# Performance work log

Hardware: AMD Instinct MI355X
Metric: run time of the kernel (lower is better)

The kernel has to match this reference:

```python
import jax, jax.numpy as jnp
import numpy as np

WS = 8          # window size
HEADS = 12      # attention heads
DIM = 768
HEAD_DIM = DIM // HEADS
EPS = 1e-5      # torch nn.LayerNorm default


def _layernorm(x, w, b):
    m = x.mean(-1, keepdims=True)
    v = ((x - m) ** 2).mean(-1, keepdims=True)
    return (x - m) / jnp.sqrt(v + EPS) * w + b


def setup_inputs() -> dict:
    key = jax.random.key(0)
    ks = jax.random.split(key, 8)
    s = 0.02  # weight init scale for numerical sanity
    dim, hd, ws = DIM, HEAD_DIM, WS
    return {
        "x": jax.random.normal(ks[0], (2, 16, 16, 16, dim), jnp.float32),
        "w_qkv": jax.random.normal(ks[1], (dim, 3 * dim), jnp.float32) * s,
        "b_qkv": jnp.zeros((3 * dim,), jnp.float32),
        "w_proj": jax.random.normal(ks[2], (dim, dim), jnp.float32) * s,
        "b_proj": jnp.zeros((dim,), jnp.float32),
        "rel_pos_d": jax.random.normal(ks[3], (2 * ws - 1, hd), jnp.float32) * s,
        "rel_pos_h": jax.random.normal(ks[4], (2 * ws - 1, hd), jnp.float32) * s,
        "rel_pos_w": jax.random.normal(ks[5], (2 * ws - 1, hd), jnp.float32) * s,
        "norm1_w": jnp.ones((dim,), jnp.float32),
        "norm1_b": jnp.zeros((dim,), jnp.float32),
        "norm2_w": jnp.ones((dim,), jnp.float32),
        "norm2_b": jnp.zeros((dim,), jnp.float32),
        "w1": jax.random.normal(ks[6], (dim, 4 * dim), jnp.float32) * s,
        "b1": jnp.zeros((4 * dim,), jnp.float32),
        "w2": jax.random.normal(ks[7], (4 * dim, dim), jnp.float32) * s,
        "b2": jnp.zeros((dim,), jnp.float32),
    }


def reference(x, w_qkv, b_qkv, w_proj, b_proj, rel_pos_d, rel_pos_h, rel_pos_w,
              norm1_w, norm1_b, norm2_w, norm2_b, w1, b1, w2, b2):
    B, D, H, W, C = x.shape
    ws, h = WS, HEADS
    hd = C // h
    scale = hd ** -0.5
    N = ws ** 3

    shortcut = x
    xn = _layernorm(x, norm1_w, norm1_b)

    # window partition (dims divide evenly -> no padding)
    xw = xn.reshape(B, D // ws, ws, H // ws, ws, W // ws, ws, C)
    xw = xw.transpose(0, 1, 3, 5, 2, 4, 6, 7).reshape(-1, N, C)  # [Bw, N, C]
    Bw = xw.shape[0]

    qkv = (xw @ w_qkv + b_qkv).reshape(Bw, N, 3, h, hd)
    qkv = qkv.transpose(2, 0, 3, 1, 4).reshape(3, Bw * h, N, hd)
    q, k, v = qkv[0], qkv[1], qkv[2]  # each [Bw*h, N, hd]

    attn = jnp.einsum('bqc,bkc->bqk', q * scale, k)  # [Bw*h, N, N]

    # decomposed relative position bias; q_size == k_size == ws, so no interp
    idx = jnp.arange(ws)[:, None] - jnp.arange(ws)[None, :] + (ws - 1)  # [ws, ws]
    Rd, Rh, Rw = rel_pos_d[idx], rel_pos_h[idx], rel_pos_w[idx]  # [ws, ws, hd]
    rq = q.reshape(Bw * h, ws, ws, ws, hd)
    rel_d = jnp.einsum('bdhwc,dkc->bdhwk', rq, Rd)
    rel_h = jnp.einsum('bdhwc,hkc->bdhwk', rq, Rh)
    rel_w = jnp.einsum('bdhwc,wkc->bdhwk', rq, Rw)
    attn = (attn.reshape(Bw * h, ws, ws, ws, ws, ws, ws)
            + rel_d[:, :, :, :, :, None, None]
            + rel_h[:, :, :, :, None, :, None]
            + rel_w[:, :, :, :, None, None, :]).reshape(Bw * h, N, N)

    attn = jax.nn.softmax(attn, axis=-1)
    out = (attn @ v).reshape(Bw, h, ws, ws, ws, hd)
    out = out.transpose(0, 2, 3, 4, 1, 5).reshape(Bw, N, C)
    out = out @ w_proj + b_proj

    # window unpartition
    out = out.reshape(B, D // ws, H // ws, W // ws, ws, ws, ws, C)
    out = out.transpose(0, 1, 4, 2, 5, 3, 6, 7).reshape(B, D, H, W, C)

    x = shortcut + out
    xn2 = _layernorm(x, norm2_w, norm2_b)
    # torch nn.GELU default is exact erf GELU
    x = x + (jax.nn.gelu(xn2 @ w1 + b1, approximate=False) @ w2 + b2)
    return x
```

## Files before the change

### kernel.cpp

```cpp
#include <hip/hip_runtime.h>
#include <hip/hip_bf16.h>
#include <math.h>

typedef short s16x8 __attribute__((ext_vector_type(8)));
typedef float f32x4 __attribute__((ext_vector_type(4)));
typedef int   s32x4 __attribute__((ext_vector_type(4)));

#define DIM 768
#define HEADS 12

static __device__ __forceinline__ short f2bf(float x) {
    union { float f; unsigned u; } v; v.f = x;
    unsigned r = (v.u + 0x7FFF + ((v.u >> 16) & 1)) >> 16;
    return (short)r;
}
static __device__ __forceinline__ float bf2f(short x) {
    union { unsigned u; float f; } v;
    v.u = ((unsigned)(unsigned short)x) << 16;
    return v.f;
}
static __device__ __forceinline__ unsigned cvt_pk_bf16(float lo, float hi) {
    unsigned r;
    asm("v_cvt_pk_bf16_f32 %0, %1, %2" : "=v"(r) : "v"(lo), "v"(hi));
    return r;
}

#define GLDS16(g, l) __builtin_amdgcn_global_load_lds( \
    (__attribute__((address_space(1))) void*)(g), \
    (__attribute__((address_space(3))) void*)(l), 16, 0, 0)

template<int Nw> static __device__ __forceinline__ void waitvm() {
    if constexpr (Nw == 8)      asm volatile("s_waitcnt vmcnt(8)" ::: "memory");
    else if constexpr (Nw == 6) asm volatile("s_waitcnt vmcnt(6)" ::: "memory");
    else if constexpr (Nw == 4) asm volatile("s_waitcnt vmcnt(4)" ::: "memory");
    else if constexpr (Nw == 3) asm volatile("s_waitcnt vmcnt(3)" ::: "memory");
    else                        asm volatile("s_waitcnt vmcnt(0)" ::: "memory");
    __builtin_amdgcn_sched_barrier(0);
}

static __device__ __forceinline__ int nat_row(int t) {
    int w = t >> 9, n = t & 511;
    int b = w >> 3, dO = (w >> 2) & 1, hO = (w >> 1) & 1, wO = w & 1;
    int di = n >> 6, hi = (n >> 3) & 7, wi = n & 7;
    int Dd = dO * 8 + di, Hh = hO * 8 + hi, Ww = wO * 8 + wi;
    return ((b * 16 + Dd) * 16 + Hh) * 16 + Ww;
}

__global__ __launch_bounds__(256) void transpose_cvt(
    const float* __restrict__ in, short* __restrict__ out, int K, int N) {
    __shared__ float tile[32][33];
    int n0 = blockIdx.x * 32, k0 = blockIdx.y * 32;
    int tx = threadIdx.x & 31, ty = threadIdx.x >> 5;
#pragma unroll
    for (int j = 0; j < 4; j++) {
        int r = ty + j * 8;
        tile[r][tx] = in[(size_t)(k0 + r) * N + n0 + tx];
    }
    __syncthreads();
#pragma unroll
    for (int j = 0; j < 4; j++) {
        int r = ty + j * 8;
        out[(size_t)(n0 + r) * K + k0 + tx] = f2bf(tile[tx][r]);
    }
}

template<int PART>
__global__ __launch_bounds__(256) void ln_kernel(
    const float* __restrict__ x, const float* __restrict__ gw,
    const float* __restrict__ gb, short* __restrict__ out) {
    int t = blockIdx.x;
    int row = PART ? nat_row(t) : t;
    const float* xr = x + (size_t)row * DIM;
    float v0 = xr[threadIdx.x], v1 = xr[threadIdx.x + 256], v2 = xr[threadIdx.x + 512];
    float s1 = v0 + v1 + v2;
    float s2 = v0 * v0 + v1 * v1 + v2 * v2;
#pragma unroll
    for (int o = 32; o > 0; o >>= 1) { s1 += __shfl_down(s1, o); s2 += __shfl_down(s2, o); }
    __shared__ float ws1[4], ws2[4];
    int wid = threadIdx.x >> 6, lane = threadIdx.x & 63;
    if (lane == 0) { ws1[wid] = s1; ws2[wid] = s2; }
    __syncthreads();
    s1 = ws1[0] + ws1[1] + ws1[2] + ws1[3];
    s2 = ws2[0] + ws2[1] + ws2[2] + ws2[3];
    float mean = s1 * (1.f / DIM);
    float var = s2 * (1.f / DIM) - mean * mean;
    float inv = rsqrtf(var + 1e-5f);
    short* orow = out + (size_t)t * DIM;
    orow[threadIdx.x]       = f2bf((v0 - mean) * inv * gw[threadIdx.x]       + gb[threadIdx.x]);
    orow[threadIdx.x + 256] = f2bf((v1 - mean) * inv * gw[threadIdx.x + 256] + gb[threadIdx.x + 256]);
    orow[threadIdx.x + 512] = f2bf((v2 - mean) * inv * gw[threadIdx.x + 512] + gb[threadIdx.x + 512]);
}

enum { EPI_C = 0, EPI_PROJ = 1, EPI_GELU = 2, EPI_MLP2 = 3 };

template<int EPI, int K, int N, int BN>
__global__ __launch_bounds__(256) void gemm_kernel(
    const short* __restrict__ A, const short* __restrict__ BT,
    const float* __restrict__ bias,
    const float* __restrict__ x_in, float* __restrict__ out_f,
    short* __restrict__ out_b) {
    constexpr int GX = N / BN;
    constexpr int GM = 64;
    constexpr int NW = BN / 32;
    constexpr int NT = K / 32;
    constexpr int LA = 2, LB = BN / 64, L = LA + LB;
    __shared__ short As[3][128 * 32];
    __shared__ short Bs[3][BN * 32];
    int flat = blockIdx.x;
    int xcd = flat & 7, idx = flat >> 3;
    constexpr int TN = GX / 2, TM = GM / 4;
    int tile_m = (xcd >> 1) * TM + idx / TN;
    int tile_n = (xcd & 1) * TN + idx % TN;
    int tid = threadIdx.x;
    int wid = tid >> 6, lane = tid & 63, lr = lane & 15, lg = lane >> 4;
    int wr = wid >> 1, wc = wid & 1;
    f32x4 acc[4][NW] = {};
    const short* Arow = A + (size_t)(tile_m * 128) * K;
    const short* Brow = BT + (size_t)(tile_n * BN) * K;
    int srcq = ((tid & 3) ^ ((tid >> 3) & 3)) * 8;
    const short* gA[LA]; const short* gB[LB];
    int ldsA[LA], ldsB[LB];
#pragma unroll
    for (int i = 0; i < LA; i++) {
        gA[i] = Arow + (size_t)(i * 64 + (tid >> 2)) * K + srcq;
        ldsA[i] = (i * 256 + wid * 64) * 8;
    }
#pragma unroll
    for (int i = 0; i < LB; i++) {
        gB[i] = Brow + (size_t)(i * 64 + (tid >> 2)) * K + srcq;
        ldsB[i] = (i * 256 + wid * 64) * 8;
    }
    auto stage = [&](int buf, int t) {
        int k0 = t * 32;
#pragma unroll
        for (int i = 0; i < LA; i++) GLDS16(gA[i] + k0, &As[buf][ldsA[i]]);
#pragma unroll
        for (int i = 0; i < LB; i++) GLDS16(gB[i] + k0, &Bs[buf][ldsB[i]]);
    };
    auto compute = [&](int buf) {
        s16x8 af[4], bfr[NW];
#pragma unroll
        for (int m = 0; m < 4; m++) {
            int row = wr * 64 + m * 16 + lr;
            af[m] = *(const s16x8*)&As[buf][row * 32 + ((lg ^ ((lr >> 1) & 3)) << 3)];
        }
#pragma unroll
        for (int n = 0; n < NW; n++) {
            int row = wc * (BN / 2) + n * 16 + lr;
            bfr[n] = *(const s16x8*)&Bs[buf][row * 32 + ((lg ^ ((lr >> 1) & 3)) << 3)];
        }
#pragma unroll
        for (int m = 0; m < 4; m++)
#pragma unroll
            for (int n = 0; n < NW; n++)
                acc[m][n] = __builtin_amdgcn_mfma_f32_16x16x32_bf16(af[m], bfr[n], acc[m][n], 0, 0, 0);
    };
    stage(0, 0); stage(1, 1);
#pragma unroll 1
    for (int tt = 0; tt < NT - 3; tt += 3) {
        stage(2, tt + 2);
        waitvm<2 * L>(); __builtin_amdgcn_s_barrier(); __builtin_amdgcn_sched_barrier(0);
        compute(0);
        __builtin_amdgcn_s_barrier();
        stage(0, tt + 3);
        waitvm<2 * L>(); __builtin_amdgcn_s_barrier(); __builtin_amdgcn_sched_barrier(0);
        compute(1);
        __builtin_amdgcn_s_barrier();
        stage(1, tt + 4);
        waitvm<2 * L>(); __builtin_amdgcn_s_barrier(); __builtin_amdgcn_sched_barrier(0);
        compute(2);
        __builtin_amdgcn_s_barrier();
    }
    stage(2, NT - 1);
    waitvm<2 * L>(); __builtin_amdgcn_s_barrier(); __builtin_amdgcn_sched_barrier(0);
    compute(0);
    __builtin_amdgcn_s_barrier();
    waitvm<L>(); __builtin_amdgcn_s_barrier(); __builtin_amdgcn_sched_barrier(0);
    compute(1);
    __builtin_amdgcn_s_barrier();
    waitvm<0>(); __builtin_amdgcn_s_barrier(); __builtin_amdgcn_sched_barrier(0);
    compute(2);
#pragma unroll
    for (int m = 0; m < 4; m++)
#pragma unroll
        for (int n = 0; n < NW; n++)
#pragma unroll
            for (int r = 0; r < 4; r++) {
                int row = tile_m * 128 + wr * 64 + m * 16 + lg * 4 + r;
                int col = tile_n * BN + wc * (BN / 2) + n * 16 + lr;
                float v = acc[m][n][r] + bias[col];
                if (EPI == EPI_C) {
                    out_b[(size_t)row * N + col] = f2bf(v);
                } else if (EPI == EPI_PROJ) {
                    int nr = nat_row(row);
                    out_f[(size_t)nr * DIM + col] = v + x_in[(size_t)nr * DIM + col];
                } else if (EPI == EPI_GELU) {
                    float u = v * (0.7978845608f + 0.0356774081f * v * v);
                    float e = __expf(2.f * u);
                    float g = v - v * __builtin_amdgcn_rcpf(1.f + e);
                    out_b[(size_t)row * (size_t)N + col] = f2bf(g);
                } else {
                    out_f[(size_t)row * DIM + col] += v;
                }
            }
}

__global__ __launch_bounds__(256) void repack_vt(
    const short* __restrict__ qkv, short* __restrict__ vt) {
    __shared__ short tile[64][72];
    int ntb = blockIdx.x, wh = blockIdx.y;
    int win = wh / HEADS, h = wh % HEADS;
    const short* vbase = qkv + (size_t)(win * 512 + ntb * 64) * 2304 + 1536 + h * 64;
    int tid = threadIdx.x;
#pragma unroll
    for (int p = 0; p < 2; p++) {
        int idx = tid + p * 256;
        int tok = idx >> 3, vc = idx & 7;
        s16x8 v = *(const s16x8*)&vbase[(size_t)tok * 2304 + vc * 8];
#pragma unroll
        for (int j = 0; j < 8; j++) tile[vc * 8 + j][tok] = v[j];
    }
    __syncthreads();
#pragma unroll
    for (int p = 0; p < 2; p++) {
        int idx = tid + p * 256;
        int d = idx >> 3, vc = idx & 7;
        s16x8 o = *(const s16x8*)&tile[d][vc * 8];
        *(s16x8*)&vt[((size_t)wh * 64 + d) * 512 + ntb * 64 + vc * 8] = o;
    }
}

__global__ __launch_bounds__(256) void attn_kernel(
    const short* __restrict__ qkv, const short* __restrict__ vt,
    const float* __restrict__ rpd, const float* __restrict__ rph,
    const float* __restrict__ rpw, short* __restrict__ out) {
    __shared__ float bdT[8][128], bhT[8][128], bwT[8][128];
    __shared__ short Rs[48 * 64];
    __shared__ short Ks[2][64 * 64];
    __shared__ short Vs[2][64 * 64];
    int qt2 = blockIdx.x;
    int wh = blockIdx.y;
    int win = wh / HEADS, h = wh % HEADS;
    int qbase = qt2 * 128;
    const short* qp = qkv + (size_t)(win * 512) * 2304 + h * 64;
    const short* kp = qp + 768;
    const short* vp = vt + (size_t)wh * 64 * 512;
    int tid = threadIdx.x, wid = tid >> 6, lane = tid & 63, lr = lane & 15, lg = lane >> 4;
    const float LOG2E = 1.4426950408889634f;

    s16x8 aq[2][2];
#pragma unroll
    for (int g = 0; g < 2; g++) {
        size_t qoff = (size_t)(qbase + g * 64 + wid * 16 + lr) * 2304;
        aq[g][0] = *(const s16x8*)&qp[qoff + lg * 8];
        aq[g][1] = *(const s16x8*)&qp[qoff + 32 + lg * 8];
    }

    for (int i = tid; i < 48 * 64; i += 256) {
        int row = i >> 6, c = i & 63;
        float v = 0.f;
        if (row < 9)                     v = rpd[(qt2 * 2 + row) * 64 + c];
        else if (row >= 16 && row < 31)  v = rph[(row - 16) * 64 + c];
        else if (row >= 32 && row < 47)  v = rpw[(row - 32) * 64 + c];
        Rs[row * 64 + ((((c >> 3) ^ (row & 7)) << 3) | (c & 7))] = f2bf(v * LOG2E);
    }
    __syncthreads();

    int row0 = wid * 8 + (lane >> 3);
    int swz = ((lane & 7) ^ (row0 & 7)) * 8;
    const short* kSrc0 = kp + (size_t)row0 * 2304 + swz;
    const short* kSrc1 = kp + (size_t)(row0 + 32) * 2304 + swz;
    const short* vSrc0 = vp + (size_t)row0 * 512 + swz;
    const short* vSrc1 = vp + (size_t)(row0 + 32) * 512 + swz;
    int ldsOff0 = wid * 512, ldsOff1 = 2048 + wid * 512;

    GLDS16(kSrc0, &Ks[0][ldsOff0]);
    GLDS16(kSrc1, &Ks[0][ldsOff1]);
    GLDS16(vSrc0, &Vs[0][ldsOff0]);
    GLDS16(vSrc1, &Vs[0][ldsOff1]);

    {
        f32x4 G[3][2];
#pragma unroll
        for (int t = 0; t < 3; t++) {
            int arow = t * 16 + lr;
            s16x8 a0 = *(const s16x8*)&Rs[arow * 64 + ((lg ^ (arow & 7)) << 3)];
            s16x8 a1 = *(const s16x8*)&Rs[arow * 64 + (((4 + lg) ^ (arow & 7)) << 3)];
#pragma unroll
            for (int g = 0; g < 2; g++) {
                f32x4 z = {};
                z = __builtin_amdgcn_mfma_f32_16x16x32_bf16(a0, aq[g][0], z, 0, 0, 0);
                z = __builtin_amdgcn_mfma_f32_16x16x32_bf16(a1, aq[g][1], z, 0, 0, 0);
                G[t][g] = z;
            }
        }
        int qcH = (wid * 2 + (lr >> 3)) & 7;
        int qcW = lr & 7;
#pragma unroll
        for (int g = 0; g < 2; g++) {
            int qr = g * 64 + wid * 16 + lr;
#pragma unroll
            for (int r = 0; r < 4; r++) {
                int j = lg * 4 + r;
                int kd = g + 7 - j;
                if (kd >= 0 && kd < 8) bdT[kd][qr] = G[0][g][r];
                int kh = qcH + 7 - j;
                if (kh >= 0 && kh < 8) bhT[kh][qr] = G[1][g][r];
                int kw = qcW + 7 - j;
                if (kw >= 0 && kw < 8) bwT[kw][qr] = G[2][g][r];
            }
        }
    }
    __syncthreads();

    float m_run[2] = {-1e30f, -1e30f}, l_run[2] = {0.f, 0.f};
    f32x4 accO[2][4] = {};
    int sel = lg >> 1;
    const float SC = 0.125f * LOG2E;

#pragma unroll 1
    for (int kt = 0; kt < 8; kt++) {
        int cur = kt & 1;
        if (kt < 7) {
            size_t kAdv = (size_t)(kt + 1) * 64 * 2304;
            int vAdv = (kt + 1) * 64;
            GLDS16(kSrc0 + kAdv, &Ks[cur ^ 1][ldsOff0]);
            GLDS16(kSrc1 + kAdv, &Ks[cur ^ 1][ldsOff1]);
            GLDS16(vSrc0 + vAdv, &Vs[cur ^ 1][ldsOff0]);
            GLDS16(vSrc1 + vAdv, &Vs[cur ^ 1][ldsOff1]);
        }
        f32x4 sa[2][4];
#pragma unroll
        for (int kn = 0; kn < 4; kn++) {
            int krow = kn * 16 + lr;
            const short* kb_ = &Ks[cur][krow * 64];
            s16x8 ak0 = *(const s16x8*)&kb_[((lg ^ (krow & 7)) << 3)];
            s16x8 ak1 = *(const s16x8*)&kb_[(((4 + lg) ^ (krow & 7)) << 3)];
#pragma unroll
            for (int g = 0; g < 2; g++) {
                f32x4 z = {};
                z = __builtin_amdgcn_mfma_f32_16x16x32_bf16(ak0, aq[g][0], z, 0, 0, 0);
                z = __builtin_amdgcn_mfma_f32_16x16x32_bf16(ak1, aq[g][1], z, 0, 0, 0);
                sa[g][kn] = z;
            }
        }
        s32x4 pb[2][2];
#pragma unroll
        for (int g = 0; g < 2; g++) {
            int qr = g * 64 + wid * 16 + lr;
            float bdv = bdT[kt][qr];
            float bb[4], bwv[4];
#pragma unroll
            for (int kn = 0; kn < 4; kn++) bb[kn] = bdv + bhT[2 * kn + sel][qr];
#pragma unroll
            for (int r = 0; r < 4; r++) bwv[r] = bwT[4 * (lg & 1) + r][qr];
            float sv[4][4], mx = -1e30f;
#pragma unroll
            for (int kn = 0; kn < 4; kn++)
#pragma unroll
                for (int r = 0; r < 4; r++) {
                    float vv = sa[g][kn][r] * SC + (bb[kn] + bwv[r]);
                    sv[kn][r] = vv;
                    mx = fmaxf(mx, vv);
                }
            mx = fmaxf(mx, __shfl_xor(mx, 16));
            mx = fmaxf(mx, __shfl_xor(mx, 32));
            float nm = fmaxf(m_run[g], mx);
            float corr = exp2f(m_run[g] - nm);
            m_run[g] = nm;
            float p[4][4], tsum = 0.f;
#pragma unroll
            for (int kn = 0; kn < 4; kn++)
#pragma unroll
                for (int r = 0; r < 4; r++) {
                    float pv = exp2f(sv[kn][r] - nm);
                    p[kn][r] = pv; tsum += pv;
                }
            tsum += __shfl_xor(tsum, 16);
            tsum += __shfl_xor(tsum, 32);
            l_run[g] = l_run[g] * corr + tsum;
#pragma unroll
            for (int n = 0; n < 4; n++)
#pragma unroll
                for (int r = 0; r < 4; r++) accO[g][n][r] *= corr;
            unsigned u[4][2];
#pragma unroll
            for (int kn = 0; kn < 4; kn++) {
                u[kn][0] = cvt_pk_bf16(p[kn][0], p[kn][1]);
                u[kn][1] = cvt_pk_bf16(p[kn][2], p[kn][3]);
            }
#pragma unroll
            for (int s2 = 0; s2 < 2; s2++)
#pragma unroll
                for (int tp = 0; tp < 2; tp++) {
                    int src = (2 * (lg & 1) + tp) * 16 + lr;
#pragma unroll
                    for (int j = 0; j < 2; j++) {
                        int a0 = __shfl((int)u[2 * s2][j], src);
                        int a1 = __shfl((int)u[2 * s2 + 1][j], src);
                        pb[g][s2][tp * 2 + j] = sel ? a1 : a0;
                    }
                }
        }
#pragma unroll
        for (int s2 = 0; s2 < 2; s2++) {
            s16x8 pb0 = *(s16x8*)&pb[0][s2];
            s16x8 pb1 = *(s16x8*)&pb[1][s2];
#pragma unroll
            for (int n = 0; n < 4; n++) {
                int vrow = n * 16 + lr;
                s16x8 av = *(const s16x8*)&Vs[cur][vrow * 64 + (((s2 * 4 + lg) ^ (vrow & 7)) << 3)];
                accO[0][n] = __builtin_amdgcn_mfma_f32_16x16x32_bf16(av, pb0, accO[0][n], 0, 0, 0);
                accO[1][n] = __builtin_amdgcn_mfma_f32_16x16x32_bf16(av, pb1, accO[1][n], 0, 0, 0);
            }
        }
        __syncthreads();
    }
#pragma unroll
    for (int g = 0; g < 2; g++) {
        float inv = __builtin_amdgcn_rcpf(l_run[g]);
        int tok = win * 512 + qbase + g * 64 + wid * 16 + lr;
        short* orow = out + (size_t)tok * DIM + h * 64;
#pragma unroll
        for (int n = 0; n < 4; n++)
#pragma unroll
            for (int j = 0; j < 2; j++) {
                unsigned uo = cvt_pk_bf16(accO[g][n][2 * j] * inv, accO[g][n][2 * j + 1] * inv);
                *(unsigned*)&orow[n * 16 + 4 * lg + 2 * j] = uo;
            }
    }
}

extern "C" void kernel_launch(void* const* d_in, const int* in_sizes, int n_in,
                              void* d_out, int out_size, void* d_ws, size_t ws_size,
                              hipStream_t stream) {
    const float* x      = (const float*)d_in[0];
    const float* w_qkv  = (const float*)d_in[1];
    const float* b_qkv  = (const float*)d_in[2];
    const float* w_proj = (const float*)d_in[3];
    const float* b_proj = (const float*)d_in[4];
    const float* rpd    = (const float*)d_in[5];
    const float* rph    = (const float*)d_in[6];
    const float* rpw    = (const float*)d_in[7];
    const float* n1w    = (const float*)d_in[8];
    const float* n1b    = (const float*)d_in[9];
    const float* n2w    = (const float*)d_in[10];
    const float* n2b    = (const float*)d_in[11];
    const float* w1     = (const float*)d_in[12];
    const float* b1     = (const float*)d_in[13];
    const float* w2     = (const float*)d_in[14];
    const float* b2     = (const float*)d_in[15];
    float* out = (float*)d_out;
    char* ws = (char*)d_ws;
    size_t off = 0;
    auto alloc = [&](size_t bytes) { void* p = ws + off; off += (bytes + 255) & ~255ULL; return p; };
    short* wqkvT  = (short*)alloc((size_t)2304 * 768 * 2);
    short* wprojT = (short*)alloc((size_t)768 * 768 * 2);
    short* w1T    = (short*)alloc((size_t)3072 * 768 * 2);
    short* w2T    = (short*)alloc((size_t)768 * 3072 * 2);
    short* xn1    = (short*)alloc((size_t)8192 * 768 * 2);
    short* qkvC   = (short*)alloc((size_t)8192 * 2304 * 2);
    short* vtb    = (short*)alloc((size_t)192 * 64 * 512 * 2);
    short* xn2    = (short*)alloc((size_t)8192 * 768 * 2);
    short* hid    = (short*)alloc((size_t)8192 * 3072 * 2);
    short* attnout = xn1;

    transpose_cvt<<<dim3(2304 / 32, 768 / 32), 256, 0, stream>>>(w_qkv, wqkvT, 768, 2304);
    transpose_cvt<<<dim3(768 / 32, 768 / 32), 256, 0, stream>>>(w_proj, wprojT, 768, 768);
    transpose_cvt<<<dim3(3072 / 32, 768 / 32), 256, 0, stream>>>(w1, w1T, 768, 3072);
    transpose_cvt<<<dim3(768 / 32, 3072 / 32), 256, 0, stream>>>(w2, w2T, 3072, 768);

    ln_kernel<1><<<8192, 256, 0, stream>>>(x, n1w, n1b, xn1);
    gemm_kernel<EPI_C, 768, 2304, 128><<<64 * 18, 256, 0, stream>>>(
        xn1, wqkvT, b_qkv, nullptr, nullptr, qkvC);
    repack_vt<<<dim3(8, 192), 256, 0, stream>>>(qkvC, vtb);
    attn_kernel<<<dim3(4, 192), 256, 0, stream>>>(qkvC, vtb, rpd, rph, rpw, attnout);
    gemm_kernel<EPI_PROJ, 768, 768, 64><<<64 * 12, 256, 0, stream>>>(
        attnout, wprojT, b_proj, x, out, nullptr);
    ln_kernel<0><<<8192, 256, 0, stream>>>(out, n2w, n2b, xn2);
    gemm_kernel<EPI_GELU, 768, 3072, 128><<<64 * 24, 256, 0, stream>>>(
        xn2, w1T, b1, nullptr, nullptr, hid);
    gemm_kernel<EPI_MLP2, 3072, 768, 64><<<64 * 12, 256, 0, stream>>>(
        hid, w2T, b2, nullptr, out, nullptr);
}
```

Measured before the change: 283.3 us.

## Replace triple-buffered GEMM pipeline with simple double-buffered loop

The GEMM main loop drops its three-buffer LDS pipeline, which used explicit vmcnt waits and split barriers. In its place is a two-buffer loop that prefetches the next K tile, computes the current one, then calls __syncthreads. This cuts shared memory per block, which may allow more resident blocks, and removes the hand-tuned wait logic. The cost is a shallower prefetch depth and a full barrier each iteration, which likely waits on all outstanding loads and exposes more memory latency.

```diff
diff --git a/kernel.cpp b/kernel.cpp
--- a/kernel.cpp
+++ b/kernel.cpp
@@ -28,15 +28,6 @@
 #define GLDS16(g, l) __builtin_amdgcn_global_load_lds( \
     (__attribute__((address_space(1))) void*)(g), \
     (__attribute__((address_space(3))) void*)(l), 16, 0, 0)
-
-template<int Nw> static __device__ __forceinline__ void waitvm() {
-    if constexpr (Nw == 8)      asm volatile("s_waitcnt vmcnt(8)" ::: "memory");
-    else if constexpr (Nw == 6) asm volatile("s_waitcnt vmcnt(6)" ::: "memory");
-    else if constexpr (Nw == 4) asm volatile("s_waitcnt vmcnt(4)" ::: "memory");
-    else if constexpr (Nw == 3) asm volatile("s_waitcnt vmcnt(3)" ::: "memory");
-    else                        asm volatile("s_waitcnt vmcnt(0)" ::: "memory");
-    __builtin_amdgcn_sched_barrier(0);
-}
 
 static __device__ __forceinline__ int nat_row(int t) {
     int w = t >> 9, n = t & 511;
@@ -103,9 +94,9 @@
     constexpr int GM = 64;
     constexpr int NW = BN / 32;
     constexpr int NT = K / 32;
-    constexpr int LA = 2, LB = BN / 64, L = LA + LB;
-    __shared__ short As[3][128 * 32];
-    __shared__ short Bs[3][BN * 32];
+    constexpr int LA = 2, LB = BN / 64;
+    __shared__ short As[2][128 * 32];
+    __shared__ short Bs[2][BN * 32];
     int flat = blockIdx.x;
     int xcd = flat & 7, idx = flat >> 3;
     constexpr int TN = GX / 2, TM = GM / 4;
@@ -137,49 +128,30 @@
 #pragma unroll
         for (int i = 0; i < LB; i++) GLDS16(gB[i] + k0, &Bs[buf][ldsB[i]]);
     };
-    auto compute = [&](int buf) {
+    stage(0, 0);
+    __syncthreads();
+#pragma unroll 1
+    for (int t = 0; t < NT; t++) {
+        int cur = t & 1;
+        if (t + 1 < NT) stage(cur ^ 1, t + 1);
         s16x8 af[4], bfr[NW];
 #pragma unroll
         for (int m = 0; m < 4; m++) {
             int row = wr * 64 + m * 16 + lr;
-            af[m] = *(const s16x8*)&As[buf][row * 32 + ((lg ^ ((lr >> 1) & 3)) << 3)];
+            af[m] = *(const s16x8*)&As[cur][row * 32 + ((lg ^ ((lr >> 1) & 3)) << 3)];
         }
 #pragma unroll
         for (int n = 0; n < NW; n++) {
             int row = wc * (BN / 2) + n * 16 + lr;
-            bfr[n] = *(const s16x8*)&Bs[buf][row * 32 + ((lg ^ ((lr >> 1) & 3)) << 3)];
+            bfr[n] = *(const s16x8*)&Bs[cur][row * 32 + ((lg ^ ((lr >> 1) & 3)) << 3)];
         }
 #pragma unroll
         for (int m = 0; m < 4; m++)
 #pragma unroll
             for (int n = 0; n < NW; n++)
                 acc[m][n] = __builtin_amdgcn_mfma_f32_16x16x32_bf16(af[m], bfr[n], acc[m][n], 0, 0, 0);
-    };
-    stage(0, 0); stage(1, 1);
-#pragma unroll 1
-    for (int tt = 0; tt < NT - 3; tt += 3) {
-        stage(2, tt + 2);
-        waitvm<2 * L>(); __builtin_amdgcn_s_barrier(); __builtin_amdgcn_sched_barrier(0);
-        compute(0);
-        __builtin_amdgcn_s_barrier();
-        stage(0, tt + 3);
-        waitvm<2 * L>(); __builtin_amdgcn_s_barrier(); __builtin_amdgcn_sched_barrier(0);
-        compute(1);
-        __builtin_amdgcn_s_barrier();
-        stage(1, tt + 4);
-        waitvm<2 * L>(); __builtin_amdgcn_s_barrier(); __builtin_amdgcn_sched_barrier(0);
-        compute(2);
-        __builtin_amdgcn_s_barrier();
-    }
-    stage(2, NT - 1);
-    waitvm<2 * L>(); __builtin_amdgcn_s_barrier(); __builtin_amdgcn_sched_barrier(0);
-    compute(0);
-    __builtin_amdgcn_s_barrier();
-    waitvm<L>(); __builtin_amdgcn_s_barrier(); __builtin_amdgcn_sched_barrier(0);
-    compute(1);
-    __builtin_amdgcn_s_barrier();
-    waitvm<0>(); __builtin_amdgcn_s_barrier(); __builtin_amdgcn_sched_barrier(0);
-    compute(2);
+        __syncthreads();
+    }
 #pragma unroll
     for (int m = 0; m < 4; m++)
 #pragma unroll
```

Result: no change. 278.5 us (-1.7%).
